# Kernel tuning notes

Hardware: AMD Instinct MI355X
Metric: run time of the kernel (lower is better)

Reference implementation:

```python
import math
import jax, jax.numpy as jnp
import numpy as np

B, N, D, H, L, TD, KN, KE = 4, 256, 512, 8, 6, 128, 16, 4
DH = D // H
EPS = 1e-5


def _ln(x, g, b):
    m = jnp.mean(x, axis=-1, keepdims=True)
    v = jnp.var(x, axis=-1, keepdims=True)
    return (x - m) * jax.lax.rsqrt(v + EPS) * g + b


def setup_inputs() -> dict:
    key = jax.random.key(0)
    ks = iter(jax.random.split(key, 64))
    s = 0.02
    inp = {
        'x_nodes_t': jax.random.randint(next(ks), (B, N), 0, KN),
        'x_edges_t': jax.random.randint(next(ks), (B, N, N), 0, KE),
        't': jax.random.randint(next(ks), (B,), 0, 1000),
        'c_emb_vec': jax.random.normal(next(ks), (B, D), jnp.float32),
        # embeddings / time MLP
        'node_embed': s * jax.random.normal(next(ks), (KN, D), jnp.float32),
        'time_w1': s * jax.random.normal(next(ks), (TD, D), jnp.float32),
        'time_b1': jnp.zeros((D,), jnp.float32),
        'time_w2': s * jax.random.normal(next(ks), (D, D), jnp.float32),
        'time_b2': jnp.zeros((D,), jnp.float32),
        'edge_bias_tab': s * jax.random.normal(next(ks), (KE, H), jnp.float32),
        # stacked per-layer params [L, ...]
        'ln1_g': jnp.ones((L, D), jnp.float32),
        'ln1_b': jnp.zeros((L, D), jnp.float32),
        'Wq': s * jax.random.normal(next(ks), (L, D, D), jnp.float32),
        'Wk': s * jax.random.normal(next(ks), (L, D, D), jnp.float32),
        'Wv': s * jax.random.normal(next(ks), (L, D, D), jnp.float32),
        'Wo': s * jax.random.normal(next(ks), (L, D, D), jnp.float32),
        'ln2_g': jnp.ones((L, D), jnp.float32),
        'ln2_b': jnp.zeros((L, D), jnp.float32),
        'ff_w1': s * jax.random.normal(next(ks), (L, D, 4 * D), jnp.float32),
        'ff_b1': jnp.zeros((L, 4 * D), jnp.float32),
        'ff_w2': s * jax.random.normal(next(ks), (L, 4 * D, D), jnp.float32),
        'ff_b2': jnp.zeros((L, D), jnp.float32),
        # output heads
        'node_w': s * jax.random.normal(next(ks), (D, KN), jnp.float32),
        'node_b': jnp.zeros((KN,), jnp.float32),
        'pair_w1': s * jax.random.normal(next(ks), (2 * D, D), jnp.float32),
        'pair_b1': jnp.zeros((D,), jnp.float32),
        'pair_w2': s * jax.random.normal(next(ks), (D, KE), jnp.float32),
        'pair_b2': jnp.zeros((KE,), jnp.float32),
    }
    return inp


def _forward(x_nodes_t, x_edges_t, t, c_emb_vec, node_embed, time_w1, time_b1,
             time_w2, time_b2, edge_bias_tab, ln1_g, ln1_b, Wq, Wk, Wv, Wo,
             ln2_g, ln2_b, ff_w1, ff_b1, ff_w2, ff_b2, node_w, node_b,
             pair_w1, pair_b1, pair_w2, pair_b2):
    # sinusoidal time embedding: [B] -> [B, TD]
    half = TD // 2
    freqs = jnp.exp(-math.log(10000.0) * jnp.arange(half, dtype=jnp.float32) / half)
    ang = t.astype(jnp.float32)[:, None] * freqs[None, :]
    temb = jnp.concatenate([jnp.sin(ang), jnp.cos(ang)], axis=-1)
    temb = jax.nn.silu(temb @ time_w1 + time_b1) @ time_w2 + time_b2  # [B, D]

    h = node_embed[x_nodes_t]                      # [B, N, D]
    h = h + temb[:, None, :] + c_emb_vec[:, None, :]

    attn_bias = jnp.transpose(edge_bias_tab[x_edges_t], (0, 3, 1, 2))  # [B, H, N, N]
    scale = DH ** -0.5

    for i in range(L):
        hn = _ln(h, ln1_g[i], ln1_b[i])
        q = (hn @ Wq[i]).reshape(B, N, H, DH)
        k = (hn @ Wk[i]).reshape(B, N, H, DH)
        v = (hn @ Wv[i]).reshape(B, N, H, DH)
        logits = jnp.einsum('bnhd,bmhd->bhnm', q, k) * scale + attn_bias
        a = jax.nn.softmax(logits, axis=-1)
        o = jnp.einsum('bhnm,bmhd->bnhd', a, v).reshape(B, N, D)
        h = h + o @ Wo[i]
        hn2 = _ln(h, ln2_g[i], ln2_b[i])
        h = h + jax.nn.silu(hn2 @ ff_w1[i] + ff_b1[i]) @ ff_w2[i] + ff_b2[i]

    node_logits = h @ node_w + node_b              # [B, N, KN]

    # edge pair MLP: concat([h_i, h_j]) @ W1 == h_i @ W1a + h_j @ W1b (fused form)
    w1a, w1b = pair_w1[:D], pair_w1[D:]
    pa = h @ w1a                                   # [B, N, D]
    pb = h @ w1b                                   # [B, N, D]
    pair = jax.nn.silu(pa[:, :, None, :] + pb[:, None, :, :] + pair_b1)  # [B,N,N,D]
    edge_logits = pair @ pair_w2 + pair_b2         # [B, N, N, KE]

    idx = jnp.arange(N)
    edge_logits = edge_logits.at[:, idx, idx, :].set(-1e9)
    edge_logits = edge_logits.at[:, idx, idx, 0].set(1e9)
    edge_logits = 0.5 * (edge_logits + jnp.transpose(edge_logits, (0, 2, 1, 3)))
    return node_logits, edge_logits


def reference(x_nodes_t, x_edges_t, t, c_emb_vec, node_embed, time_w1, time_b1,
              time_w2, time_b2, edge_bias_tab, ln1_g, ln1_b, Wq, Wk, Wv, Wo,
              ln2_g, ln2_b, ff_w1, ff_b1, ff_w2, ff_b2, node_w, node_b,
              pair_w1, pair_b1, pair_w2, pair_b2):
    return _forward(x_nodes_t, x_edges_t, t, c_emb_vec, node_embed, time_w1,
                    time_b1, time_w2, time_b2, edge_bias_tab, ln1_g, ln1_b,
                    Wq, Wk, Wv, Wo, ln2_g, ln2_b, ff_w1, ff_b1, ff_w2, ff_b2,
                    node_w, node_b, pair_w1, pair_b1, pair_w2, pair_b2)
```

## Files before the change

kernel.cpp:

```cpp
#include <hip/hip_runtime.h>
#include <math.h>

#define BB 4
#define NN 256
#define DD 512
#define HH 8
#define LL 6
#define TDIM 128
#define KNN 16
#define KEE 4
#define DHH 64
#define PSTRIDE ((size_t)BB * NN * NN * KEE)

typedef unsigned short u16;
typedef __bf16 bf16x8 __attribute__((ext_vector_type(8)));
typedef float f32x16 __attribute__((ext_vector_type(16)));
typedef u16 u16x8 __attribute__((ext_vector_type(8)));
typedef u16 u16x4 __attribute__((ext_vector_type(4)));
typedef unsigned int u32;

#define GLOBAL_AS(p) ((__attribute__((address_space(1))) void*)(p))
#define LDS_AS(p)    ((__attribute__((address_space(3))) void*)(p))

__device__ __forceinline__ u16 f2bf(float x) {
    unsigned u = __float_as_uint(x);
    u = (u + 0x7FFFu + ((u >> 16) & 1u)) >> 16;
    return (u16)u;
}
__device__ __forceinline__ float bf2f(u16 x) {
    return __uint_as_float(((unsigned)x) << 16);
}
__device__ __forceinline__ u32 cvtpk_bf16(float lo, float hi) {
    u32 r;
    asm("v_cvt_pk_bf16_f32 %0, %1, %2" : "=v"(r) : "v"(lo), "v"(hi));
    return r;
}

__global__ void temb_kernel(const int* __restrict__ t_in, const float* __restrict__ w1,
                            const float* __restrict__ b1, const float* __restrict__ w2,
                            const float* __restrict__ b2, float* __restrict__ temb)
{
    int b = blockIdx.x;
    int t = threadIdx.x;
    __shared__ float t0[TDIM];
    __shared__ float t1[DD];
    float tv = (float)t_in[b];
    if (t < TDIM) {
        int j = t & 63;
        float fr = expf(-logf(10000.f) * (float)j / 64.f);
        float ang = tv * fr;
        t0[t] = (t < 64) ? sinf(ang) : cosf(ang);
    }
    __syncthreads();
    float acc = b1[t];
    for (int k = 0; k < TDIM; ++k) acc += t0[k] * w1[k * DD + t];
    t1[t] = acc / (1.f + expf(-acc));
    __syncthreads();
    float acc2 = b2[t];
    for (int k = 0; k < DD; ++k) acc2 += t1[k] * w2[k * DD + t];
    temb[b * DD + t] = acc2;
}

__global__ void inith_kernel(const int* __restrict__ xn, const float* __restrict__ ne,
                             const float* __restrict__ temb, const float* __restrict__ cemb,
                             float* __restrict__ h)
{
    int idx = blockIdx.x * 256 + threadIdx.x;
    int d = idx & (DD - 1);
    int bn = idx >> 9;
    int b = bn >> 8;
    h[idx] = ne[xn[bn] * DD + d] + temb[b * DD + d] + cemb[b * DD + d];
}

__global__ __launch_bounds__(256) void ln_kernel(const float* __restrict__ x,
                                                 const float* __restrict__ g,
                                                 const float* __restrict__ bta,
                                                 u16* __restrict__ y)
{
    int row = blockIdx.x;
    const float* xr = x + (size_t)row * DD;
    int t = threadIdx.x;
    float v0 = xr[t], v1 = xr[t + 256];
    float s = v0 + v1, sq = v0 * v0 + v1 * v1;
    #pragma unroll
    for (int o = 32; o; o >>= 1) { s += __shfl_down(s, o); sq += __shfl_down(sq, o); }
    __shared__ float ss[4], sqs[4];
    __shared__ float mean_s, rstd_s;
    int w = t >> 6, lane = t & 63;
    if (!lane) { ss[w] = s; sqs[w] = sq; }
    __syncthreads();
    if (t == 0) {
        float S = ss[0] + ss[1] + ss[2] + ss[3];
        float Q = sqs[0] + sqs[1] + sqs[2] + sqs[3];
        float m = S / DD;
        float var = Q / DD - m * m;
        mean_s = m; rstd_s = rsqrtf(var + 1e-5f);
    }
    __syncthreads();
    float m = mean_s, r = rstd_s;
    y[(size_t)row * DD + t]       = f2bf((v0 - m) * r * g[t] + bta[t]);
    y[(size_t)row * DD + t + 256] = f2bf((v1 - m) * r * g[t + 256] + bta[t + 256]);
}

struct CvtSeg { const float* src; u16* dst; int K, N, tx, ty, nl, base; };
struct CvtTab { CvtSeg s[8]; };

__global__ __launch_bounds__(256) void convert_all(CvtTab tab)
{
    const int tile = blockIdx.x;
    int si = 0;
    #pragma unroll
    for (int s2 = 1; s2 < 8; ++s2) if (tile >= tab.s[s2].base) si = s2;
    const CvtSeg sg = tab.s[si];
    int local = tile - sg.base;
    int per = sg.tx * sg.ty;
    int lay = local / per;
    int rem = local - lay * per;
    int bx = rem % sg.tx, by = rem / sg.tx;
    const int kb = by * 64, nb = bx * 64;
    const size_t zoff = (size_t)lay * sg.K * sg.N;
    const int K = sg.K, N = sg.N;

    __shared__ float s[64][65];
    int t = threadIdx.x;
    int r0 = t >> 4, c0 = (t & 15) * 4;
    #pragma unroll
    for (int i = 0; i < 4; ++i) {
        int row = i * 16 + r0;
        float4 v = *reinterpret_cast<const float4*>(sg.src + zoff + (size_t)(kb + row) * N + nb + c0);
        s[row][c0] = v.x; s[row][c0 + 1] = v.y; s[row][c0 + 2] = v.z; s[row][c0 + 3] = v.w;
    }
    __syncthreads();
    #pragma unroll
    for (int i = 0; i < 4; ++i) {
        int n = i * 16 + r0;
        ushort4 o;
        o.x = f2bf(s[c0 + 0][n]); o.y = f2bf(s[c0 + 1][n]);
        o.z = f2bf(s[c0 + 2][n]); o.w = f2bf(s[c0 + 3][n]);
        *reinterpret_cast<ushort4*>(sg.dst + zoff + (size_t)(nb + n) * K + kb + c0) = o;
    }
}

template<int WM, int WN, int NR, int KS, bool BIAS, bool SILU, bool RES, bool OBF, bool HBF>
__global__ __launch_bounds__(WM * WN * 64 * KS) void gemm_mfma(
    const u16* __restrict__ A,
    const u16* __restrict__ B0, const u16* __restrict__ B1, const u16* __restrict__ B2,
    const float* __restrict__ bias, const float* res,
    void* O0, void* O1, void* O2, u16* hbf,
    int M, int N, int K)
{
    constexpr int BM = WM * 32, BN = WN * NR * 32;
    constexpr int GW = WM * WN;
    constexpr int TH = GW * 64;
    constexpr int ABYTES = BM * 128;
    constexpr int BBYTES = BN * 128;
    constexpr int A16 = ABYTES / 16;
    constexpr int B16 = BBYTES / 16;
    __shared__ char smem[KS * 2 * (ABYTES + BBYTES)];

    const u16* Bm = B0; void* O = O0;
    if (blockIdx.z == 1) { Bm = B1; O = O1; }
    else if (blockIdx.z == 2) { Bm = B2; O = O2; }

    const int t = threadIdx.x;
    const int l = t & 63;
    const int w = t >> 6;
    const int ks = w / GW;
    const int wsub = w - ks * GW;
    const int tl = wsub * 64 + l;
    const int lo = l & 31, hi = l >> 5;
    const int wm = wsub / WN, wn = wsub % WN;
    const int row0 = blockIdx.y * BM;
    const int col0 = blockIdx.x * BN;
    const int NK = K >> 6;
    const int NKh = NK / KS;

    char* gbase = smem + ks * 2 * (ABYTES + BBYTES);

    int aoff[4];
    int boff[NR][4];
    #pragma unroll
    for (int kc = 0; kc < 4; ++kc) {
        int slot = (kc * 2 + hi) ^ (lo & 7);
        aoff[kc] = (wm * 32 + lo) * 128 + slot * 16;
        #pragma unroll
        for (int nr = 0; nr < NR; ++nr)
            boff[nr][kc] = (wn * NR * 32 + nr * 32 + lo) * 128 + slot * 16;
    }

    auto stage = [&](int buf, int kt) {
        const int k0 = kt * 64;
        char* base = gbase + buf * (ABYTES + BBYTES);
        #pragma unroll
        for (int idx = tl; idx < A16; idx += TH) {
            int r = idx >> 3, s = idx & 7;
            int ss = s ^ (r & 7);
            const u16* g = A + (size_t)(row0 + r) * K + k0 + ss * 8;
            __builtin_amdgcn_global_load_lds(GLOBAL_AS(g), LDS_AS(base + (idx - l) * 16), 16, 0, 0);
        }
        #pragma unroll
        for (int idx = tl; idx < B16; idx += TH) {
            int r = idx >> 3, s = idx & 7;
            int ss = s ^ (r & 7);
            const u16* g = Bm + (size_t)(col0 + r) * K + k0 + ss * 8;
            __builtin_amdgcn_global_load_lds(GLOBAL_AS(g), LDS_AS(base + ABYTES + (idx - l) * 16), 16, 0, 0);
        }
    };

    f32x16 acc[NR];
    #pragma unroll
    for (int nr = 0; nr < NR; ++nr)
        #pragma unroll
        for (int i = 0; i < 16; ++i) acc[nr][i] = 0.f;

    stage(0, ks * NKh);
    __syncthreads();
    int cur = 0;
    for (int kk = 0; kk < NKh; ++kk) {
        if (kk + 1 < NKh) stage(cur ^ 1, ks * NKh + kk + 1);
        const char* base = gbase + cur * (ABYTES + BBYTES);
        #pragma unroll
        for (int kc = 0; kc < 4; ++kc) {
            bf16x8 av = *reinterpret_cast<const bf16x8*>(base + aoff[kc]);
            #pragma unroll
            for (int nr = 0; nr < NR; ++nr) {
                bf16x8 bb = *reinterpret_cast<const bf16x8*>(base + ABYTES + boff[nr][kc]);
                acc[nr] = __builtin_amdgcn_mfma_f32_32x32x16_bf16(av, bb, acc[nr], 0, 0, 0);
            }
        }
        __syncthreads();
        cur ^= 1;
    }

    if (KS > 1) {
        float* exch = (float*)smem;
        if (ks > 0) {
            #pragma unroll
            for (int nr = 0; nr < NR; ++nr)
                #pragma unroll
                for (int r = 0; r < 16; ++r)
                    exch[(((ks - 1) * NR + nr) * 16 + r) * TH + tl] = acc[nr][r];
        }
        __syncthreads();
        if (ks != 0) return;
        #pragma unroll
        for (int g2 = 1; g2 < KS; ++g2)
            #pragma unroll
            for (int nr = 0; nr < NR; ++nr)
                #pragma unroll
                for (int r = 0; r < 16; ++r)
                    acc[nr][r] += exch[(((g2 - 1) * NR + nr) * 16 + r) * TH + tl];
    }

    #pragma unroll
    for (int nr = 0; nr < NR; ++nr) {
        int col = col0 + wn * NR * 32 + nr * 32 + lo;
        float bs = BIAS ? bias[col] : 0.f;
        #pragma unroll
        for (int r = 0; r < 16; ++r) {
            int row = row0 + wm * 32 + (r & 3) + 8 * (r >> 2) + 4 * hi;
            float v = acc[nr][r] + bs;
            if (SILU) v = v / (1.f + __expf(-v));
            size_t o = (size_t)row * N + col;
            if (RES) v += res[o];
            if (OBF) ((u16*)O)[o] = f2bf(v);
            else { ((float*)O)[o] = v; if (HBF) hbf[o] = f2bf(v); }
        }
    }
}

__global__ __launch_bounds__(256) void attn_kernel(
    const u16* __restrict__ q8, const u16* __restrict__ k8, const u16* __restrict__ v8,
    const int* __restrict__ xe, const float* __restrict__ tab, u16* __restrict__ o)
{
    const int qt = blockIdx.x * 32, hh = blockIdx.y, b = blockIdx.z;
    const int t = threadIdx.x;
    const int l = t & 63, w = t >> 6;
    const int lo = l & 31, hi = l >> 5;

    __shared__ u16 Ks[NN * 64];
    __shared__ u16 Qs[32 * 64];
    __shared__ u16 Vt[64 * NN];
    __shared__ float opart[4][32 * 64];
    __shared__ float sums[4][32];
    __shared__ float tabs[KEE * HH];

    #pragma unroll
    for (int c = 0; c < 8; ++c) {
        int idx = c * 256 + t;
        int r = idx >> 3, s = idx & 7;
        int ss = s ^ (r & 7);
        const u16* g = k8 + ((size_t)(b * NN + r) * HH + hh) * DHH + ss * 8;
        __builtin_amdgcn_global_load_lds(GLOBAL_AS(g), LDS_AS((char*)Ks + (idx - l) * 16), 16, 0, 0);
    }
    {
        int r = t >> 3, s = t & 7;
        int ss = s ^ (r & 7);
        const u16* g = q8 + ((size_t)(b * NN + qt + r) * HH + hh) * DHH + ss * 8;
        __builtin_amdgcn_global_load_lds(GLOBAL_AS(g), LDS_AS((char*)Qs + (t - l) * 16), 16, 0, 0);
    }
    if (t < KEE * HH) tabs[t] = tab[t];

    {
        const int d0 = (t & 7) * 8, k0 = (t >> 3) * 8;
        u16x8 va[8];
        #pragma unroll
        for (int i = 0; i < 8; ++i)
            va[i] = *reinterpret_cast<const u16x8*>(v8 + ((size_t)(b * NN + k0 + i) * HH + hh) * DHH + d0);
        #pragma unroll
        for (int j = 0; j < 8; ++j) {
            u16x8 tj;
            #pragma unroll
            for (int i = 0; i < 8; ++i) tj[i] = va[i][j];
            int d = d0 + j;
            int slot = (k0 >> 3) ^ (d & 31);
            *reinterpret_cast<u16x8*>(&Vt[d * 256 + slot * 8]) = tj;
        }
    }
    __syncthreads();

    f32x16 acc[2];
    #pragma unroll
    for (int i = 0; i < 2; ++i)
        #pragma unroll
        for (int r = 0; r < 16; ++r) acc[i][r] = 0.f;

    #pragma unroll
    for (int kc = 0; kc < 4; ++kc) {
        int qslot = (kc * 2 + hi) ^ (lo & 7);
        bf16x8 bq = *reinterpret_cast<const bf16x8*>((char*)Qs + lo * 128 + qslot * 16);
        #pragma unroll
        for (int ktl = 0; ktl < 2; ++ktl) {
            int key = (2 * w + ktl) * 32 + lo;
            int kslot = (kc * 2 + hi) ^ (key & 7);
            bf16x8 ak = *reinterpret_cast<const bf16x8*>((char*)Ks + key * 128 + kslot * 16);
            acc[ktl] = __builtin_amdgcn_mfma_f32_32x32x16_bf16(ak, bq, acc[ktl], 0, 0, 0);
        }
    }

    const int qrow = qt + lo;
    const int* xerow = xe + (size_t)(b * NN + qrow) * NN;
    float psum = 0.f;
    #pragma unroll
    for (int ktl = 0; ktl < 2; ++ktl) {
        #pragma unroll
        for (int r = 0; r < 16; ++r) {
            int key = w * 64 + ktl * 32 + (r & 3) + 8 * (r >> 2) + 4 * hi;
            int e = xerow[key];
            float p = __expf(acc[ktl][r] * 0.125f + tabs[e * HH + hh]);
            acc[ktl][r] = p;
            psum += p;
        }
    }
    psum += __shfl_xor(psum, 32);
    if (hi == 0) sums[w][lo] = psum;

    f32x16 oacc[2];
    #pragma unroll
    for (int i = 0; i < 2; ++i)
        #pragma unroll
        for (int r = 0; r < 16; ++r) oacc[i][r] = 0.f;

    #pragma unroll
    for (int kc = 0; kc < 4; ++kc) {
        const int ai = kc >> 1;
        const int s0 = 8 * (kc & 1);
        u32 W0p = cvtpk_bf16(acc[ai][s0 + 0], acc[ai][s0 + 1]);
        u32 W1p = cvtpk_bf16(acc[ai][s0 + 2], acc[ai][s0 + 3]);
        u32 X0p = cvtpk_bf16(acc[ai][s0 + 4], acc[ai][s0 + 5]);
        u32 X1p = cvtpk_bf16(acc[ai][s0 + 6], acc[ai][s0 + 7]);
        u32 z0 = hi ? W0p : X0p;
        u32 z1 = hi ? W1p : X1p;
        u32 r0 = __shfl_xor((int)z0, 32);
        u32 r1 = __shfl_xor((int)z1, 32);
        u32 F[4];
        F[0] = hi ? r0 : W0p;
        F[1] = hi ? r1 : W1p;
        F[2] = hi ? X0p : r0;
        F[3] = hi ? X1p : r1;
        bf16x8 pf = *reinterpret_cast<const bf16x8*>(F);
        #pragma unroll
        for (int nt = 0; nt < 2; ++nt) {
            int d = nt * 32 + lo;
            int slot = (8 * w + kc * 2 + hi) ^ (d & 31);
            bf16x8 vf = *reinterpret_cast<const bf16x8*>(&Vt[d * 256 + slot * 8]);
            oacc[nt] = __builtin_amdgcn_mfma_f32_32x32x16_bf16(pf, vf, oacc[nt], 0, 0, 0);
        }
    }

    #pragma unroll
    for (int nt = 0; nt < 2; ++nt)
        #pragma unroll
        for (int r = 0; r < 16; ++r) {
            int q = (r & 3) + 8 * (r >> 2) + 4 * hi;
            opart[w][q * 64 + nt * 32 + lo] = oacc[nt][r];
        }
    __syncthreads();

    {
        const int q = t >> 3, dd0 = (t & 7) * 8;
        float denom = sums[0][q] + sums[1][q] + sums[2][q] + sums[3][q];
        float rc = __builtin_amdgcn_rcpf(denom);
        u16x8 o8;
        #pragma unroll
        for (int j = 0; j < 8; ++j) {
            float s = opart[0][q * 64 + dd0 + j] + opart[1][q * 64 + dd0 + j]
                    + opart[2][q * 64 + dd0 + j] + opart[3][q * 64 + dd0 + j];
            o8[j] = f2bf(s * rc);
        }
        *reinterpret_cast<u16x8*>(o + ((size_t)(b * NN + qt + q) * HH + hh) * DHH + dd0) = o8;
    }
}

__global__ __launch_bounds__(256) void nodelogits_kernel(const float* __restrict__ h,
                                                         const float* __restrict__ nw,
                                                         const float* __restrict__ nb,
                                                         float* __restrict__ out)
{
    int row = blockIdx.x;
    int t = threadIdx.x;
    int kk = t & 15, seg = t >> 4;
    const float* hr = h + (size_t)row * DD;
    float acc = 0.f;
    #pragma unroll 8
    for (int d = seg * 32; d < seg * 32 + 32; ++d) acc += hr[d] * nw[d * KNN + kk];
    __shared__ float sm[16][17];
    sm[seg][kk] = acc;
    __syncthreads();
    if (t < KNN) {
        float s = 0.f;
        #pragma unroll
        for (int g2 = 0; g2 < 16; ++g2) s += sm[g2][t];
        out[(size_t)row * KNN + t] = s + nb[t];
    }
}

__global__ __launch_bounds__(256) void pair_kernel(
    const u16* __restrict__ pa8, const u16* __restrict__ pb8,
    const float* __restrict__ b1, const float* __restrict__ w2,
    float* __restrict__ etmp)
{
    const int jt = blockIdx.x * 32, it = blockIdx.y * 32;
    const int b = blockIdx.z >> 1, half = blockIdx.z & 1;
    const int t = threadIdx.x;
    const int j2 = t & 15, i2 = t >> 4;

    __shared__ float pas[32][132];
    __shared__ float pbs[32][132];
    __shared__ float4 w2s[128];

    float4 acc00 = {0,0,0,0}, acc01 = {0,0,0,0}, acc10 = {0,0,0,0}, acc11 = {0,0,0,0};

    for (int c2 = 0; c2 < 2; ++c2) {
        const int d0 = (half * 2 + c2) * 128;
        if (c2) __syncthreads();
        #pragma unroll
        for (int c = 0; c < 2; ++c) {
            int qd = c * 256 + t;
            int r = qd >> 4, part = (qd & 15) * 8;
            u16x8 av = *reinterpret_cast<const u16x8*>(pa8 + (size_t)(b * NN + it + r) * DD + d0 + part);
            u16x8 bv = *reinterpret_cast<const u16x8*>(pb8 + (size_t)(b * NN + jt + r) * DD + d0 + part);
            float4 b1a = *reinterpret_cast<const float4*>(b1 + d0 + part);
            float4 b1b = *reinterpret_cast<const float4*>(b1 + d0 + part + 4);
            *reinterpret_cast<float4*>(&pas[r][part]) =
                make_float4(bf2f(av[0]) + b1a.x, bf2f(av[1]) + b1a.y, bf2f(av[2]) + b1a.z, bf2f(av[3]) + b1a.w);
            *reinterpret_cast<float4*>(&pas[r][part + 4]) =
                make_float4(bf2f(av[4]) + b1b.x, bf2f(av[5]) + b1b.y, bf2f(av[6]) + b1b.z, bf2f(av[7]) + b1b.w);
            *reinterpret_cast<float4*>(&pbs[r][part]) =
                make_float4(bf2f(bv[0]), bf2f(bv[1]), bf2f(bv[2]), bf2f(bv[3]));
            *reinterpret_cast<float4*>(&pbs[r][part + 4]) =
                make_float4(bf2f(bv[4]), bf2f(bv[5]), bf2f(bv[6]), bf2f(bv[7]));
        }
        if (t < 128) w2s[t] = *reinterpret_cast<const float4*>(w2 + (size_t)(d0 + t) * KEE);
        __syncthreads();

        #pragma unroll 4
        for (int dq = 0; dq < 32; ++dq) {
            float4 paA = *reinterpret_cast<const float4*>(&pas[i2][dq * 4]);
            float4 paB = *reinterpret_cast<const float4*>(&pas[i2 + 16][dq * 4]);
            float4 pbA = *reinterpret_cast<const float4*>(&pbs[j2][dq * 4]);
            float4 pbB = *reinterpret_cast<const float4*>(&pbs[j2 + 16][dq * 4]);
            float4 w0 = w2s[dq * 4], w1 = w2s[dq * 4 + 1], w2v = w2s[dq * 4 + 2], w3 = w2s[dq * 4 + 3];

            #define HSILU(x) ((x) * __builtin_amdgcn_fmed3f(__builtin_fmaf((x), 0.25f, 0.5f), 0.f, 1.f))
            #define PAIR_STEP(ACC, PA, PB)                                                     \
            {                                                                                  \
                float s0 = HSILU(PA.x + PB.x), s1 = HSILU(PA.y + PB.y);                        \
                float s2 = HSILU(PA.z + PB.z), s3 = HSILU(PA.w + PB.w);                        \
                ACC.x += s0 * w0.x + s1 * w1.x + s2 * w2v.x + s3 * w3.x;                       \
                ACC.y += s0 * w0.y + s1 * w1.y + s2 * w2v.y + s3 * w3.y;                       \
                ACC.z += s0 * w0.z + s1 * w1.z + s2 * w2v.z + s3 * w3.z;                       \
                ACC.w += s0 * w0.w + s1 * w1.w + s2 * w2v.w + s3 * w3.w;                       \
            }
            PAIR_STEP(acc00, paA, pbA)
            PAIR_STEP(acc01, paA, pbB)
            PAIR_STEP(acc10, paB, pbA)
            PAIR_STEP(acc11, paB, pbB)
            #undef PAIR_STEP
            #undef HSILU
        }
    }

    float* ep = etmp + half * PSTRIDE;
    #define WRITE(ACC, I, J)                                                                   \
        *reinterpret_cast<float4*>(ep + (((size_t)(b * NN + (I)) * NN) + (J)) * KEE) =         \
            make_float4(ACC.x, ACC.y, ACC.z, ACC.w);
    WRITE(acc00, it + i2,      jt + j2)
    WRITE(acc01, it + i2,      jt + j2 + 16)
    WRITE(acc10, it + i2 + 16, jt + j2)
    WRITE(acc11, it + i2 + 16, jt + j2 + 16)
    #undef WRITE
}

__global__ void symm_kernel(const float* __restrict__ et, const float* __restrict__ b2,
                            float* __restrict__ out)
{
    int idx = blockIdx.x * 256 + threadIdx.x;
    int j = idx & 255;
    int i = (idx >> 8) & 255;
    int b = idx >> 16;
    size_t fwd = (size_t)idx * KEE;
    size_t rev = (((size_t)b * NN + j) * NN + i) * KEE;
    float4 r4;
    if (i == j) {
        r4 = make_float4(1e9f, -1e9f, -1e9f, -1e9f);
    } else {
        float4 a0 = *reinterpret_cast<const float4*>(et + fwd);
        float4 a1 = *reinterpret_cast<const float4*>(et + PSTRIDE + fwd);
        float4 c0 = *reinterpret_cast<const float4*>(et + rev);
        float4 c1 = *reinterpret_cast<const float4*>(et + PSTRIDE + rev);
        r4 = make_float4(0.5f * (a0.x + a1.x + c0.x + c1.x) + b2[0],
                         0.5f * (a0.y + a1.y + c0.y + c1.y) + b2[1],
                         0.5f * (a0.z + a1.z + c0.z + c1.z) + b2[2],
                         0.5f * (a0.w + a1.w + c0.w + c1.w) + b2[3]);
    }
    *reinterpret_cast<float4*>(out + (size_t)BB * NN * KNN + fwd) = r4;
}

extern "C" void kernel_launch(void* const* d_in, const int* in_sizes, int n_in,
                              void* d_out, int out_size, void* d_ws, size_t ws_size,
                              hipStream_t stream)
{
    const int*   xn   = (const int*)d_in[0];
    const int*   xe   = (const int*)d_in[1];
    const int*   tt   = (const int*)d_in[2];
    const float* cemb = (const float*)d_in[3];
    const float* ne   = (const float*)d_in[4];
    const float* tw1  = (const float*)d_in[5];
    const float* tb1  = (const float*)d_in[6];
    const float* tw2  = (const float*)d_in[7];
    const float* tb2  = (const float*)d_in[8];
    const float* tab  = (const float*)d_in[9];
    const float* ln1g = (const float*)d_in[10];
    const float* ln1b = (const float*)d_in[11];
    const float* Wq   = (const float*)d_in[12];
    const float* Wk   = (const float*)d_in[13];
    const float* Wv   = (const float*)d_in[14];
    const float* Wo   = (const float*)d_in[15];
    const float* ln2g = (const float*)d_in[16];
    const float* ln2b = (const float*)d_in[17];
    const float* fw1  = (const float*)d_in[18];
    const float* fb1  = (const float*)d_in[19];
    const float* fw2  = (const float*)d_in[20];
    const float* fb2  = (const float*)d_in[21];
    const float* nw   = (const float*)d_in[22];
    const float* nb   = (const float*)d_in[23];
    const float* pw1  = (const float*)d_in[24];
    const float* pb1  = (const float*)d_in[25];
    const float* pw2  = (const float*)d_in[26];
    const float* pb2  = (const float*)d_in[27];
    float* out = (float*)d_out;

    char* wsb = (char*)d_ws;
    size_t off = 0;
    auto alloc = [&](size_t bytes) { char* p = wsb + off; off += (bytes + 255) & ~(size_t)255; return p; };

    float* temb = (float*)alloc(BB * DD * 4);
    float* h    = (float*)alloc((size_t)BB * NN * DD * 4);
    u16* hbf    = (u16*)alloc((size_t)BB * NN * DD * 2);
    u16* pa8    = (u16*)alloc((size_t)BB * NN * DD * 2);
    u16* pb8    = (u16*)alloc((size_t)BB * NN * DD * 2);
    u16* q8     = (u16*)alloc((size_t)BB * NN * DD * 2);
    u16* k8     = (u16*)alloc((size_t)BB * NN * DD * 2);
    u16* v8     = (u16*)alloc((size_t)BB * NN * DD * 2);
    u16* hn_bf  = (u16*)alloc((size_t)BB * NN * DD * 2);
    u16* obf    = (u16*)alloc((size_t)BB * NN * DD * 2);
    u16* ff_bf  = (u16*)alloc((size_t)BB * NN * 4 * DD * 2);
    float* et   = (float*)alloc(2 * PSTRIDE * 4);
    u16* wqT    = (u16*)alloc((size_t)LL * DD * DD * 2);
    u16* wkT    = (u16*)alloc((size_t)LL * DD * DD * 2);
    u16* wvT    = (u16*)alloc((size_t)LL * DD * DD * 2);
    u16* woT    = (u16*)alloc((size_t)LL * DD * DD * 2);
    u16* fw1T   = (u16*)alloc((size_t)LL * DD * 4 * DD * 2);
    u16* fw2T   = (u16*)alloc((size_t)LL * DD * 4 * DD * 2);
    u16* pw1aT  = (u16*)alloc((size_t)DD * DD * 2);
    u16* pw1bT  = (u16*)alloc((size_t)DD * DD * 2);

    const int M = BB * NN;

    CvtTab tb;
    tb.s[0] = { Wq,  wqT,  DD,     DD,     8,  8,  LL, 0    };
    tb.s[1] = { Wk,  wkT,  DD,     DD,     8,  8,  LL, 384  };
    tb.s[2] = { Wv,  wvT,  DD,     DD,     8,  8,  LL, 768  };
    tb.s[3] = { Wo,  woT,  DD,     DD,     8,  8,  LL, 1152 };
    tb.s[4] = { fw1, fw1T, DD,     4 * DD, 32, 8,  LL, 1536 };
    tb.s[5] = { fw2, fw2T, 4 * DD, DD,     8,  32, LL, 3072 };
    tb.s[6] = { pw1,                   pw1aT, DD, DD, 8, 8, 1, 4608 };
    tb.s[7] = { pw1 + (size_t)DD * DD, pw1bT, DD, DD, 8, 8, 1, 4672 };
    convert_all<<<4736, 256, 0, stream>>>(tb);

    temb_kernel<<<BB, DD, 0, stream>>>(tt, tw1, tb1, tw2, tb2, temb);
    inith_kernel<<<(BB * NN * DD) / 256, 256, 0, stream>>>(xn, ne, temb, cemb, h);

    for (int l = 0; l < LL; ++l) {
        size_t wo512 = (size_t)l * DD * DD;
        size_t wo2k  = (size_t)l * DD * 4 * DD;
        ln_kernel<<<M, 256, 0, stream>>>(h, ln1g + l * DD, ln1b + l * DD, hn_bf);
        gemm_mfma<2, 2, 2, 2, false, false, false, true, false><<<dim3(DD / 128, M / 64, 3), 512, 0, stream>>>(
            hn_bf, wqT + wo512, wkT + wo512, wvT + wo512, nullptr, nullptr,
            q8, k8, v8, nullptr, M, DD, DD);
        attn_kernel<<<dim3(8, HH, BB), 256, 0, stream>>>(q8, k8, v8, xe, tab, obf);
        gemm_mfma<1, 2, 1, 2, false, false, true, false, false><<<dim3(DD / 64, M / 32, 1), 256, 0, stream>>>(
            obf, woT + wo512, nullptr, nullptr, nullptr, h,
            h, nullptr, nullptr, nullptr, M, DD, DD);
        ln_kernel<<<M, 256, 0, stream>>>(h, ln2g + l * DD, ln2b + l * DD, hn_bf);
        gemm_mfma<2, 2, 2, 2, true, true, false, true, false><<<dim3(4 * DD / 128, M / 64, 1), 512, 0, stream>>>(
            hn_bf, fw1T + wo2k, nullptr, nullptr, fb1 + (size_t)l * 4 * DD, nullptr,
            ff_bf, nullptr, nullptr, nullptr, M, 4 * DD, DD);
        if (l == LL - 1)
            gemm_mfma<1, 2, 1, 2, true, false, true, false, true><<<dim3(DD / 64, M / 32, 1), 256, 0, stream>>>(
                ff_bf, fw2T + wo2k, nullptr, nullptr, fb2 + (size_t)l * DD, h,
                h, nullptr, nullptr, hbf, M, DD, 4 * DD);
        else
            gemm_mfma<1, 2, 1, 2, true, false, true, false, false><<<dim3(DD / 64, M / 32, 1), 256, 0, stream>>>(
                ff_bf, fw2T + wo2k, nullptr, nullptr, fb2 + (size_t)l * DD, h,
                h, nullptr, nullptr, nullptr, M, DD, 4 * DD);
    }

    nodelogits_kernel<<<M, 256, 0, stream>>>(h, nw, nb, out);

    gemm_mfma<1, 2, 1, 2, false, false, false, true, false><<<dim3(DD / 64, M / 32, 2), 256, 0, stream>>>(
        hbf, pw1aT, pw1bT, nullptr, nullptr, nullptr,
        pa8, pb8, nullptr, nullptr, M, DD, DD);

    pair_kernel<<<dim3(8, 8, BB * 2), 256, 0, stream>>>(pa8, pb8, pb1, pw2, et);
    symm_kernel<<<(BB * NN * NN) / 256, 256, 0, stream>>>(et, pb2, out);

    (void)in_sizes; (void)n_in; (void)out_size; (void)ws_size;
}
```

Baseline: 428.2 us.

## Fold LayerNorm into following GEMMs via precomputed weight row sums

Removes the separate LayerNorm kernels. The gamma scale is folded into the transposed bf16 weights, and per-column sums of gamma*W and beta*W are precomputed with atomics during weight conversion. Each QKV and FF1 GEMM now computes per-row mean and rstd from the bf16 residual copy in its prologue and applies the correction in the epilogue. The residual GEMMs also write a bf16 copy of h for this purpose. This saves 12 launches and the normalized-activation round trip, but it adds a redundant stats pass in every GEMM block, and computing stats from bf16 data in a single pass may cost precision.

Result: slower. 441.3 us (+3.1%).

```diff
diff --git a/kernel.cpp b/kernel.cpp
--- a/kernel.cpp
+++ b/kernel.cpp
@@ -63,46 +63,19 @@
 
 __global__ void inith_kernel(const int* __restrict__ xn, const float* __restrict__ ne,
                              const float* __restrict__ temb, const float* __restrict__ cemb,
-                             float* __restrict__ h)
+                             float* __restrict__ h, u16* __restrict__ hbf)
 {
     int idx = blockIdx.x * 256 + threadIdx.x;
     int d = idx & (DD - 1);
     int bn = idx >> 9;
     int b = bn >> 8;
-    h[idx] = ne[xn[bn] * DD + d] + temb[b * DD + d] + cemb[b * DD + d];
-}
-
-__global__ __launch_bounds__(256) void ln_kernel(const float* __restrict__ x,
-                                                 const float* __restrict__ g,
-                                                 const float* __restrict__ bta,
-                                                 u16* __restrict__ y)
-{
-    int row = blockIdx.x;
-    const float* xr = x + (size_t)row * DD;
-    int t = threadIdx.x;
-    float v0 = xr[t], v1 = xr[t + 256];
-    float s = v0 + v1, sq = v0 * v0 + v1 * v1;
-    #pragma unroll
-    for (int o = 32; o; o >>= 1) { s += __shfl_down(s, o); sq += __shfl_down(sq, o); }
-    __shared__ float ss[4], sqs[4];
-    __shared__ float mean_s, rstd_s;
-    int w = t >> 6, lane = t & 63;
-    if (!lane) { ss[w] = s; sqs[w] = sq; }
-    __syncthreads();
-    if (t == 0) {
-        float S = ss[0] + ss[1] + ss[2] + ss[3];
-        float Q = sqs[0] + sqs[1] + sqs[2] + sqs[3];
-        float m = S / DD;
-        float var = Q / DD - m * m;
-        mean_s = m; rstd_s = rsqrtf(var + 1e-5f);
-    }
-    __syncthreads();
-    float m = mean_s, r = rstd_s;
-    y[(size_t)row * DD + t]       = f2bf((v0 - m) * r * g[t] + bta[t]);
-    y[(size_t)row * DD + t + 256] = f2bf((v1 - m) * r * g[t + 256] + bta[t + 256]);
-}
-
-struct CvtSeg { const float* src; u16* dst; int K, N, tx, ty, nl, base; };
+    float v = ne[xn[bn] * DD + d] + temb[b * DD + d] + cemb[b * DD + d];
+    h[idx] = v;
+    hbf[idx] = f2bf(v);
+}
+
+struct CvtSeg { const float* src; u16* dst; const float* g; const float* b;
+                float* u; float* v; int K, N, tx, ty, nl, base; };
 struct CvtTab { CvtSeg s[8]; };
 
 __global__ __launch_bounds__(256) void convert_all(CvtTab tab)
@@ -122,6 +95,8 @@
     const int K = sg.K, N = sg.N;
 
     __shared__ float s[64][65];
+    __shared__ float redu[4][64];
+    __shared__ float redv[4][64];
     int t = threadIdx.x;
     int r0 = t >> 4, c0 = (t & 15) * 4;
     #pragma unroll
@@ -131,20 +106,54 @@
         s[row][c0] = v.x; s[row][c0 + 1] = v.y; s[row][c0 + 2] = v.z; s[row][c0 + 3] = v.w;
     }
     __syncthreads();
-    #pragma unroll
-    for (int i = 0; i < 4; ++i) {
-        int n = i * 16 + r0;
-        ushort4 o;
-        o.x = f2bf(s[c0 + 0][n]); o.y = f2bf(s[c0 + 1][n]);
-        o.z = f2bf(s[c0 + 2][n]); o.w = f2bf(s[c0 + 3][n]);
-        *reinterpret_cast<ushort4*>(sg.dst + zoff + (size_t)(nb + n) * K + kb + c0) = o;
-    }
-}
-
-template<int WM, int WN, int NR, int KS, bool BIAS, bool SILU, bool RES, bool OBF, bool HBF>
+
+    if (sg.g) {
+        const float* gp = sg.g + lay * DD + kb;
+        const float* bp = sg.b + lay * DD + kb;
+        #pragma unroll
+        for (int i = 0; i < 4; ++i) {
+            int n = i * 16 + r0;
+            ushort4 o;
+            o.x = f2bf(s[c0 + 0][n] * gp[c0 + 0]); o.y = f2bf(s[c0 + 1][n] * gp[c0 + 1]);
+            o.z = f2bf(s[c0 + 2][n] * gp[c0 + 2]); o.w = f2bf(s[c0 + 3][n] * gp[c0 + 3]);
+            *reinterpret_cast<ushort4*>(sg.dst + zoff + (size_t)(nb + n) * K + kb + c0) = o;
+        }
+        int col = t & 63, seg = t >> 6;
+        float us = 0.f, vs = 0.f;
+        #pragma unroll
+        for (int r = 0; r < 16; ++r) {
+            int row = seg * 16 + r;
+            float w_ = s[row][col];
+            us += gp[row] * w_;
+            vs += bp[row] * w_;
+        }
+        redu[seg][col] = us;
+        redv[seg][col] = vs;
+        __syncthreads();
+        if (seg == 0) {
+            float ut = redu[0][col] + redu[1][col] + redu[2][col] + redu[3][col];
+            float vt = redv[0][col] + redv[1][col] + redv[2][col] + redv[3][col];
+            atomicAdd(sg.u + (size_t)lay * N + nb + col, ut);
+            atomicAdd(sg.v + (size_t)lay * N + nb + col, vt);
+        }
+    } else {
+        #pragma unroll
+        for (int i = 0; i < 4; ++i) {
+            int n = i * 16 + r0;
+            ushort4 o;
+            o.x = f2bf(s[c0 + 0][n]); o.y = f2bf(s[c0 + 1][n]);
+            o.z = f2bf(s[c0 + 2][n]); o.w = f2bf(s[c0 + 3][n]);
+            *reinterpret_cast<ushort4*>(sg.dst + zoff + (size_t)(nb + n) * K + kb + c0) = o;
+        }
+    }
+}
+
+template<int WM, int WN, int NR, int KS, int MODE, bool BIAS, bool SILU, bool RES, bool OBF, bool HBF>
 __global__ __launch_bounds__(WM * WN * 64 * KS) void gemm_mfma(
     const u16* __restrict__ A,
     const u16* __restrict__ B0, const u16* __restrict__ B1, const u16* __restrict__ B2,
+    const float* __restrict__ u0, const float* __restrict__ u1, const float* __restrict__ u2,
+    const float* __restrict__ v0, const float* __restrict__ v1, const float* __restrict__ v2,
     const float* __restrict__ bias, const float* res,
     void* O0, void* O1, void* O2, u16* hbf,
     int M, int N, int K)
@@ -157,10 +166,12 @@
     constexpr int A16 = ABYTES / 16;
     constexpr int B16 = BBYTES / 16;
     __shared__ char smem[KS * 2 * (ABYTES + BBYTES)];
+    __shared__ float statS[MODE == 1 ? BM : 1][2];
 
     const u16* Bm = B0; void* O = O0;
-    if (blockIdx.z == 1) { Bm = B1; O = O1; }
-    else if (blockIdx.z == 2) { Bm = B2; O = O2; }
+    const float* Uv = u0; const float* Vv = v0;
+    if (blockIdx.z == 1) { Bm = B1; O = O1; Uv = u1; Vv = v1; }
+    else if (blockIdx.z == 2) { Bm = B2; O = O2; Uv = u2; Vv = v2; }
 
     const int t = threadIdx.x;
     const int l = t & 63;
@@ -175,6 +186,26 @@
     const int NK = K >> 6;
     const int NKh = NK / KS;
 
+    if constexpr (MODE == 1) {
+        const int rr = t >> 3, sub = t & 7;
+        const u16* hr = A + (size_t)(row0 + rr) * K + sub * 64;
+        float s = 0.f, sq = 0.f;
+        #pragma unroll
+        for (int c = 0; c < 8; ++c) {
+            u16x8 hv = *reinterpret_cast<const u16x8*>(hr + c * 8);
+            #pragma unroll
+            for (int e = 0; e < 8; ++e) { float x = bf2f(hv[e]); s += x; sq += x * x; }
+        }
+        #pragma unroll
+        for (int o = 1; o < 8; o <<= 1) { s += __shfl_xor(s, o); sq += __shfl_xor(sq, o); }
+        if (sub == 0) {
+            float m = s / (float)K;
+            float var = sq / (float)K - m * m;
+            statS[rr][0] = m;
+            statS[rr][1] = rsqrtf(var + 1e-5f);
+        }
+    }
+
     char* gbase = smem + ks * 2 * (ABYTES + BBYTES);
 
     int aoff[4];
@@ -256,15 +287,21 @@
     for (int nr = 0; nr < NR; ++nr) {
         int col = col0 + wn * NR * 32 + nr * 32 + lo;
         float bs = BIAS ? bias[col] : 0.f;
+        float uu = 0.f, vvv = 0.f;
+        if constexpr (MODE == 1) { uu = Uv[col]; vvv = Vv[col]; }
         #pragma unroll
         for (int r = 0; r < 16; ++r) {
-            int row = row0 + wm * 32 + (r & 3) + 8 * (r >> 2) + 4 * hi;
-            float v = acc[nr][r] + bs;
-            if (SILU) v = v / (1.f + __expf(-v));
+            int lr = wm * 32 + (r & 3) + 8 * (r >> 2) + 4 * hi;
+            int row = row0 + lr;
+            float val = acc[nr][r];
+            if constexpr (MODE == 1)
+                val = statS[lr][1] * (val - statS[lr][0] * uu) + vvv;
+            val += bs;
+            if (SILU) val = val / (1.f + __expf(-val));
             size_t o = (size_t)row * N + col;
-            if (RES) v += res[o];
-            if (OBF) ((u16*)O)[o] = f2bf(v);
-            else { ((float*)O)[o] = v; if (HBF) hbf[o] = f2bf(v); }
+            if (RES) val += res[o];
+            if (OBF) ((u16*)O)[o] = f2bf(val);
+            else { ((float*)O)[o] = val; if (HBF) hbf[o] = f2bf(val); }
         }
     }
 }
@@ -583,7 +620,6 @@
     u16* q8     = (u16*)alloc((size_t)BB * NN * DD * 2);
     u16* k8     = (u16*)alloc((size_t)BB * NN * DD * 2);
     u16* v8     = (u16*)alloc((size_t)BB * NN * DD * 2);
-    u16* hn_bf  = (u16*)alloc((size_t)BB * NN * DD * 2);
     u16* obf    = (u16*)alloc((size_t)BB * NN * DD * 2);
     u16* ff_bf  = (u16*)alloc((size_t)BB * NN * 4 * DD * 2);
     float* et   = (float*)alloc(2 * PSTRIDE * 4);
@@ -595,53 +631,64 @@
     u16* fw2T   = (u16*)alloc((size_t)LL * DD * 4 * DD * 2);
     u16* pw1aT  = (u16*)alloc((size_t)DD * DD * 2);
     u16* pw1bT  = (u16*)alloc((size_t)DD * DD * 2);
+    float* uq   = (float*)alloc((size_t)LL * DD * 4);
+    float* vq   = (float*)alloc((size_t)LL * DD * 4);
+    float* uk   = (float*)alloc((size_t)LL * DD * 4);
+    float* vk   = (float*)alloc((size_t)LL * DD * 4);
+    float* uvv  = (float*)alloc((size_t)LL * DD * 4);
+    float* vvv  = (float*)alloc((size_t)LL * DD * 4);
+    float* uf1  = (float*)alloc((size_t)LL * 4 * DD * 4);
+    float* vf1  = (float*)alloc((size_t)LL * 4 * DD * 4);
 
     const int M = BB * NN;
 
+    size_t foldBytes = (size_t)(6 * LL * DD + 2 * LL * 4 * DD) * 4 + 8 * 256;
+    hipMemsetAsync(uq, 0, foldBytes, stream);
+
     CvtTab tb;
-    tb.s[0] = { Wq,  wqT,  DD,     DD,     8,  8,  LL, 0    };
-    tb.s[1] = { Wk,  wkT,  DD,     DD,     8,  8,  LL, 384  };
-    tb.s[2] = { Wv,  wvT,  DD,     DD,     8,  8,  LL, 768  };
-    tb.s[3] = { Wo,  woT,  DD,     DD,     8,  8,  LL, 1152 };
-    tb.s[4] = { fw1, fw1T, DD,     4 * DD, 32, 8,  LL, 1536 };
-    tb.s[5] = { fw2, fw2T, 4 * DD, DD,     8,  32, LL, 3072 };
-    tb.s[6] = { pw1,                   pw1aT, DD, DD, 8, 8, 1, 4608 };
-    tb.s[7] = { pw1 + (size_t)DD * DD, pw1bT, DD, DD, 8, 8, 1, 4672 };
+    tb.s[0] = { Wq,  wqT,  ln1g, ln1b, uq,  vq,  DD,     DD,     8,  8,  LL, 0    };
+    tb.s[1] = { Wk,  wkT,  ln1g, ln1b, uk,  vk,  DD,     DD,     8,  8,  LL, 384  };
+    tb.s[2] = { Wv,  wvT,  ln1g, ln1b, uvv, vvv, DD,     DD,     8,  8,  LL, 768  };
+    tb.s[3] = { Wo,  woT,  nullptr, nullptr, nullptr, nullptr, DD, DD, 8, 8, LL, 1152 };
+    tb.s[4] = { fw1, fw1T, ln2g, ln2b, uf1, vf1, DD,     4 * DD, 32, 8,  LL, 1536 };
+    tb.s[5] = { fw2, fw2T, nullptr, nullptr, nullptr, nullptr, 4 * DD, DD, 8, 32, LL, 3072 };
+    tb.s[6] = { pw1,                   pw1aT, nullptr, nullptr, nullptr, nullptr, DD, DD, 8, 8, 1, 4608 };
+    tb.s[7] = { pw1 + (size_t)DD * DD, pw1bT, nullptr, nullptr, nullptr, nullptr, DD, DD, 8, 8, 1, 4672 };
     convert_all<<<4736, 256, 0, stream>>>(tb);
 
     temb_kernel<<<BB, DD, 0, stream>>>(tt, tw1, tb1, tw2, tb2, temb);
-    inith_kernel<<<(BB * NN * DD) / 256, 256, 0, stream>>>(xn, ne, temb, cemb, h);
+    inith_kernel<<<(BB * NN * DD) / 256, 256, 0, stream>>>(xn, ne, temb, cemb, h, hbf);
 
     for (int l = 0; l < LL; ++l) {
         size_t wo512 = (size_t)l * DD * DD;
         size_t wo2k  = (size_t)l * DD * 4 * DD;
-        ln_kernel<<<M, 256, 0, stream>>>(h, ln1g + l * DD, ln1b + l * DD, hn_bf);
-        gemm_mfma<2, 2, 2, 2, false, false, false, true, false><<<dim3(DD / 128, M / 64, 3), 512, 0, stream>>>(
-            hn_bf, wqT + wo512, wkT + wo512, wvT + wo512, nullptr, nullptr,
-            q8, k8, v8, nullptr, M, DD, DD);
+        gemm_mfma<2, 2, 2, 2, 1, false, false, false, true, false><<<dim3(DD / 128, M / 64, 3), 512, 0, stream>>>(
+            hbf, wqT + wo512, wkT + wo512, wvT + wo512,
+            uq + l * DD, uk + l * DD, uvv + l * DD,
+            vq + l * DD, vk + l * DD, vvv + l * DD,
+            nullptr, nullptr, q8, k8, v8, nullptr, M, DD, DD);
         attn_kernel<<<dim3(8, HH, BB), 256, 0, stream>>>(q8, k8, v8, xe, tab, obf);
-        gemm_mfma<1, 2, 1, 2, false, false, true, false, false><<<dim3(DD / 64, M / 32, 1), 256, 0, stream>>>(
-            obf, woT + wo512, nullptr, nullptr, nullptr, h,
-            h, nullptr, nullptr, nullptr, M, DD, DD);
-        ln_kernel<<<M, 256, 0, stream>>>(h, ln2g + l * DD, ln2b + l * DD, hn_bf);
-        gemm_mfma<2, 2, 2, 2, true, true, false, true, false><<<dim3(4 * DD / 128, M / 64, 1), 512, 0, stream>>>(
-            hn_bf, fw1T + wo2k, nullptr, nullptr, fb1 + (size_t)l * 4 * DD, nullptr,
-            ff_bf, nullptr, nullptr, nullptr, M, 4 * DD, DD);
-        if (l == LL - 1)
-            gemm_mfma<1, 2, 1, 2, true, false, true, false, true><<<dim3(DD / 64, M / 32, 1), 256, 0, stream>>>(
-                ff_bf, fw2T + wo2k, nullptr, nullptr, fb2 + (size_t)l * DD, h,
-                h, nullptr, nullptr, hbf, M, DD, 4 * DD);
-        else
-            gemm_mfma<1, 2, 1, 2, true, false, true, false, false><<<dim3(DD / 64, M / 32, 1), 256, 0, stream>>>(
-                ff_bf, fw2T + wo2k, nullptr, nullptr, fb2 + (size_t)l * DD, h,
-                h, nullptr, nullptr, nullptr, M, DD, 4 * DD);
+        gemm_mfma<1, 2, 1, 2, 0, false, false, true, false, true><<<dim3(DD / 64, M / 32, 1), 256, 0, stream>>>(
+            obf, woT + wo512, nullptr, nullptr,
+            nullptr, nullptr, nullptr, nullptr, nullptr, nullptr,
+            nullptr, h, h, nullptr, nullptr, hbf, M, DD, DD);
+        gemm_mfma<2, 2, 2, 2, 1, true, true, false, true, false><<<dim3(4 * DD / 128, M / 64, 1), 512, 0, stream>>>(
+            hbf, fw1T + wo2k, nullptr, nullptr,
+            uf1 + (size_t)l * 4 * DD, nullptr, nullptr,
+            vf1 + (size_t)l * 4 * DD, nullptr, nullptr,
+            fb1 + (size_t)l * 4 * DD, nullptr, ff_bf, nullptr, nullptr, nullptr, M, 4 * DD, DD);
+        gemm_mfma<1, 2, 1, 2, 0, true, false, true, false, true><<<dim3(DD / 64, M / 32, 1), 256, 0, stream>>>(
+            ff_bf, fw2T + wo2k, nullptr, nullptr,
+            nullptr, nullptr, nullptr, nullptr, nullptr, nullptr,
+            fb2 + (size_t)l * DD, h, h, nullptr, nullptr, hbf, M, DD, 4 * DD);
     }
 
     nodelogits_kernel<<<M, 256, 0, stream>>>(h, nw, nb, out);
 
-    gemm_mfma<1, 2, 1, 2, false, false, false, true, false><<<dim3(DD / 64, M / 32, 2), 256, 0, stream>>>(
-        hbf, pw1aT, pw1bT, nullptr, nullptr, nullptr,
-        pa8, pb8, nullptr, nullptr, M, DD, DD);
+    gemm_mfma<1, 2, 1, 2, 0, false, false, false, true, false><<<dim3(DD / 64, M / 32, 2), 256, 0, stream>>>(
+        hbf, pw1aT, pw1bT, nullptr,
+        nullptr, nullptr, nullptr, nullptr, nullptr, nullptr,
+        nullptr, nullptr, pa8, pb8, nullptr, nullptr, M, DD, DD);
 
     pair_kernel<<<dim3(8, 8, BB * 2), 256, 0, stream>>>(pa8, pb8, pb1, pw2, et);
     symm_kernel<<<(BB * NN * NN) / 256, 256, 0, stream>>>(et, pb2, out);
```
